# Performance work log

Hardware: AMD Instinct MI355X
Metric: run time of the kernel (lower is better)

## Reference

```python
import jax, jax.numpy as jnp
import numpy as np
import math

EPS = 1e-5


def _layernorm(x, gamma, beta):
    mu = jnp.mean(x, axis=-1, keepdims=True)
    var = jnp.mean(jnp.square(x - mu), axis=-1, keepdims=True)
    return (x - mu) * jax.lax.rsqrt(var + EPS) * gamma + beta


def setup_inputs() -> dict:
    key = jax.random.key(0)
    ks = jax.random.split(key, 8)
    B, Sq, Sk, D = 2, 2048, 2048, 1024
    s = 1.0 / math.sqrt(D)
    return {
        "Q": jax.random.normal(ks[0], (B, Sq, D), jnp.float32),
        "K": jax.random.normal(ks[1], (B, Sk, D), jnp.float32),
        "Wq": jax.random.normal(ks[2], (D, D), jnp.float32) * s,
        "bq": jnp.zeros((D,), jnp.float32),
        "Wk": jax.random.normal(ks[3], (D, D), jnp.float32) * s,
        "bk": jnp.zeros((D,), jnp.float32),
        "Wv": jax.random.normal(ks[4], (D, D), jnp.float32) * s,
        "bv": jnp.zeros((D,), jnp.float32),
        "Wo": jax.random.normal(ks[5], (D, D), jnp.float32) * s,
        "bo": jnp.zeros((D,), jnp.float32),
        "g0": jnp.ones((D,), jnp.float32),
        "b0": jnp.zeros((D,), jnp.float32),
        "g1": jnp.ones((D,), jnp.float32),
        "b1": jnp.zeros((D,), jnp.float32),
    }


def reference(Q, K, Wq, bq, Wk, bk, Wv, bv, Wo, bo, g0, b0, g1, b1):
    H = 16
    B, Sq, D = Q.shape
    dh = D // H
    Qp = Q @ Wq + bq                      # [B,Sq,D]
    Kp = K @ Wk + bk                      # [B,Sk,D]
    # Faithful to source: fc_v is applied to the ALREADY-projected K
    Vp = Kp @ Wv + bv                     # [B,Sk,D]
    # split heads: [B,S,H,dh] -> [B,H,S,dh]
    Qh = Qp.reshape(B, Sq, H, dh).transpose(0, 2, 1, 3)
    Kh = Kp.reshape(B, -1, H, dh).transpose(0, 2, 1, 3)
    Vh = Vp.reshape(B, -1, H, dh).transpose(0, 2, 1, 3)
    scores = jnp.einsum("bhqd,bhkd->bhqk", Qh, Kh) / math.sqrt(dh)
    attn = jax.nn.softmax(scores, axis=-1)  # dropout is identity in eval mode
    Oh = Qh + jnp.einsum("bhqk,bhkd->bhqd", attn, Vh)
    O = Oh.transpose(0, 2, 1, 3).reshape(B, Sq, D)
    O = _layernorm(O, g0, b0)
    O = O + jax.nn.gelu(O @ Wo + bo, approximate=False)
    O = _layernorm(O, g1, b1)
    return O
```

## Files before the change

### kernel.cpp

```cpp
#include <hip/hip_runtime.h>
#include <hip/hip_bf16.h>

typedef __attribute__((ext_vector_type(8))) short short8;
typedef __attribute__((ext_vector_type(4))) float f32x4;
typedef __attribute__((ext_vector_type(8))) unsigned short ushort8;

__device__ __forceinline__ unsigned short f32_to_bf16(float f) {
  return __builtin_bit_cast(unsigned short, __float2bfloat16(f));
}
__device__ __forceinline__ float bf16_to_f32(unsigned short u) {
  return __builtin_bit_cast(float, (unsigned)u << 16);
}

__device__ __forceinline__ void gload_lds16(const unsigned short* g, unsigned short* l) {
  __builtin_amdgcn_global_load_lds((const __attribute__((address_space(1))) void*)g,
                                   (__attribute__((address_space(3))) void*)l, 16, 0, 0);
}

__global__ __launch_bounds__(256) void transpose4_kernel(const float* __restrict__ W0,
                                                         const float* __restrict__ W1,
                                                         const float* __restrict__ W2,
                                                         const float* __restrict__ W3,
                                                         unsigned short* __restrict__ T0,
                                                         unsigned short* __restrict__ T1,
                                                         unsigned short* __restrict__ T2,
                                                         unsigned short* __restrict__ T3) {
  __shared__ float t[32][33];
  const int D = 1024;
  const float* Ws[4] = {W0, W1, W2, W3};
  unsigned short* Ts[4] = {T0, T1, T2, T3};
  const float* W = Ws[blockIdx.z];
  unsigned short* WT = Ts[blockIdx.z];
  int bx = blockIdx.x, by = blockIdx.y;
  int tx = threadIdx.x, ty = threadIdx.y;
#pragma unroll
  for (int i = 0; i < 4; ++i)
    t[ty * 4 + i][tx] = W[(size_t)(by * 32 + ty * 4 + i) * D + bx * 32 + tx];
  __syncthreads();
#pragma unroll
  for (int i = 0; i < 4; ++i) {
    int r = ty * 4 + i;
    WT[(size_t)(bx * 32 + r) * D + by * 32 + tx] = f32_to_bf16(t[tx][r]);
  }
}

template <bool GELU_RES, bool A_F32, int BK>
__device__ __forceinline__ void gemm_body(const void* __restrict__ Av,
                                          const unsigned short* __restrict__ Bt,
                                          const float* __restrict__ bias,
                                          const unsigned short* __restrict__ res16,
                                          float* __restrict__ out32,
                                          unsigned short* __restrict__ out16,
                                          unsigned short* __restrict__ outT,
                                          float o16_scale,
                                          int M, int N, int K,
                                          unsigned short* As, unsigned short* Bs) {
  const int tid = threadIdx.x;
  const int lane = tid & 63, wid = tid >> 6;
  const int wm = wid >> 2, wn = wid & 3;
  const int m0 = blockIdx.x * 64, n0 = blockIdx.y * 128;
  const int lr = lane & 15, lg = lane >> 4;
  const int xs = lr & 7;
  const int CPR = BK / 8;
  f32x4 acc[2][2] = {};
  for (int kt = 0; kt < K; kt += BK) {
#pragma unroll
    for (int i = 0; i < (128 * CPR) / 512; ++i) {
      int c = tid + i * 512;
      int r = c / CPR, pc = c % CPR;
      int lc = (pc & ~7) | ((pc & 7) ^ (r & 7));
      gload_lds16(Bt + (size_t)(n0 + r) * K + kt + lc * 8, Bs + c * 8);
    }
#pragma unroll
    for (int i = 0; i < (64 * CPR) / 512; ++i) {
      int c = tid + i * 512;
      int r = c / CPR, pc = c % CPR;
      int lc = (pc & ~7) | ((pc & 7) ^ (r & 7));
      if (A_F32) {
        const float* src = (const float*)Av + (size_t)(m0 + r) * K + kt + lc * 8;
        float4 f0 = *(const float4*)(src);
        float4 f1 = *(const float4*)(src + 4);
        ushort8 o;
        o[0] = f32_to_bf16(f0.x); o[1] = f32_to_bf16(f0.y);
        o[2] = f32_to_bf16(f0.z); o[3] = f32_to_bf16(f0.w);
        o[4] = f32_to_bf16(f1.x); o[5] = f32_to_bf16(f1.y);
        o[6] = f32_to_bf16(f1.z); o[7] = f32_to_bf16(f1.w);
        *(ushort8*)(As + c * 8) = o;
      } else {
        gload_lds16((const unsigned short*)Av + (size_t)(m0 + r) * K + kt + lc * 8,
                    As + c * 8);
      }
    }
    __syncthreads();
#pragma unroll
    for (int ks = 0; ks < BK / 32; ++ks) {
      short8 af[2], bfr[2];
      int ch = ks * 4 + lg;
      int chs = (ch & ~7) | ((ch & 7) ^ xs);
#pragma unroll
      for (int mf = 0; mf < 2; ++mf)
        af[mf] = *(const short8*)(As + (wm * 32 + mf * 16 + lr) * BK + (chs << 3));
#pragma unroll
      for (int nf = 0; nf < 2; ++nf)
        bfr[nf] = *(const short8*)(Bs + (wn * 32 + nf * 16 + lr) * BK + (chs << 3));
#pragma unroll
      for (int mf = 0; mf < 2; ++mf)
#pragma unroll
        for (int nf = 0; nf < 2; ++nf)
          acc[mf][nf] = __builtin_amdgcn_mfma_f32_16x16x32_bf16(af[mf], bfr[nf], acc[mf][nf], 0, 0, 0);
    }
    __syncthreads();
  }
#pragma unroll
  for (int nf = 0; nf < 2; ++nf) {
    int cn = n0 + wn * 32 + nf * 16 + lr;
    float bv = bias[cn];
#pragma unroll
    for (int mf = 0; mf < 2; ++mf) {
      int rm0 = m0 + wm * 32 + mf * 16 + lg * 4;
      float vv[4];
#pragma unroll
      for (int j = 0; j < 4; ++j) {
        float v = acc[mf][nf][j] + bv;
        if (GELU_RES) {
          float g = 0.5f * v * (1.0f + erff(v * 0.70710678118f));
          v = bf16_to_f32(res16[(size_t)(rm0 + j) * N + cn]) + g;
        }
        vv[j] = v;
        if (out32) out32[(size_t)(rm0 + j) * N + cn] = v;
        if (out16) out16[(size_t)(rm0 + j) * N + cn] = f32_to_bf16(v * o16_scale);
      }
      if (outT) {
        int bb = rm0 >> 11, kk = rm0 & 2047;
        int hh = cn >> 6, dd = cn & 63;
        int kin = kk & 63, kb = kk & ~63;
        int nfk = kin >> 4, lgk = (kin >> 2) & 3;
        int kperm = kb + (nfk >> 1) * 32 + lgk * 8 + (nfk & 1) * 4;
        ushort4 tv;
        tv.x = f32_to_bf16(vv[0]); tv.y = f32_to_bf16(vv[1]);
        tv.z = f32_to_bf16(vv[2]); tv.w = f32_to_bf16(vv[3]);
        *(ushort4*)(outT + ((size_t)((bb * 16 + hh) * 64 + dd)) * 2048 + kperm) = tv;
      }
    }
  }
}

template <bool GELU_RES>
__global__ __launch_bounds__(512) void gemm_kernel(const unsigned short* __restrict__ A,
                                                   const unsigned short* __restrict__ Bt,
                                                   const float* __restrict__ bias,
                                                   const unsigned short* __restrict__ res16,
                                                   float* __restrict__ out32,
                                                   unsigned short* __restrict__ out16,
                                                   unsigned short* __restrict__ outT,
                                                   int M, int N, int K) {
  __shared__ unsigned short As[64 * 128];
  __shared__ unsigned short Bs[128 * 128];
  gemm_body<GELU_RES, false, 128>(A, Bt, bias, res16, out32, out16, outT, 1.0f,
                                  M, N, K, As, Bs);
}

__global__ __launch_bounds__(512) void gemm_qk_kernel(const float* __restrict__ A0,
                                                      const float* __restrict__ A1,
                                                      const unsigned short* __restrict__ B0,
                                                      const unsigned short* __restrict__ B1,
                                                      const float* __restrict__ bias0,
                                                      const float* __restrict__ bias1,
                                                      unsigned short* __restrict__ o16_0,
                                                      unsigned short* __restrict__ o16_1,
                                                      int M, int N, int K) {
  __shared__ unsigned short As[64 * 64];
  __shared__ unsigned short Bs[128 * 64];
  int z = blockIdx.z;
  const float SCALE2 = 0.125f * 1.44269504089f;
  gemm_body<false, true, 64>(z ? (const void*)A1 : (const void*)A0, z ? B1 : B0,
                             z ? bias1 : bias0, nullptr,
                             nullptr, z ? o16_1 : o16_0, nullptr,
                             z ? 1.0f : SCALE2, M, N, K, As, Bs);
}

__global__ __launch_bounds__(512) void attn_kernel(const unsigned short* __restrict__ Qp,
                                                   const unsigned short* __restrict__ Kp,
                                                   const unsigned short* __restrict__ VpT,
                                                   unsigned short* __restrict__ O) {
  const int S = 2048, D = 1024;
  __shared__ unsigned short Ks[128 * 64];
  __shared__ unsigned short Vs[64 * 128];
  const int id = blockIdx.x;
  const int swz = (id & 7) * 64 + (id >> 3);
  const int bh = swz >> 4, qt = swz & 15;
  const int b = bh >> 4, h = bh & 15;
  const int tid = threadIdx.x, lane = tid & 63, w = tid >> 6;
  const int lr = lane & 15, lg = lane >> 4;
  const int xs = lr & 7;
  const size_t base = (size_t)(b * S) * D + h * 64;
  const size_t vbase = (size_t)(bh * 64) * S;
  const int q0 = qt * 128 + w * 16;
  const float INV_SCALE2 = 1.0f / (0.125f * 1.44269504089f);

  short8 qf[2];
#pragma unroll
  for (int ks = 0; ks < 2; ++ks)
    qf[ks] = *(const short8*)(Qp + base + (size_t)(q0 + lr) * D + ks * 32 + lg * 8);

  f32x4 oacc[4] = {};
  float m2 = -1e30f, lsum = 0.f;

  for (int kt = 0; kt < S; kt += 128) {
#pragma unroll
    for (int i = 0; i < 2; ++i) {
      int c = tid + i * 512;
      int rk = c >> 3, pck = c & 7;
      int lck = pck ^ (rk & 7);
      gload_lds16(Kp + base + (size_t)(kt + rk) * D + lck * 8, Ks + c * 8);
      int rv = c >> 4, pcv = c & 15;
      int lcv = (pcv & 8) | ((pcv & 7) ^ (rv & 7));
      gload_lds16(VpT + vbase + (size_t)rv * S + kt + lcv * 8, Vs + c * 8);
    }
    __syncthreads();

    f32x4 sacc[8];
#pragma unroll
    for (int nf = 0; nf < 8; ++nf) sacc[nf] = (f32x4){0.f, 0.f, 0.f, 0.f};
    __builtin_amdgcn_s_setprio(1);
#pragma unroll
    for (int ks = 0; ks < 2; ++ks) {
#pragma unroll
      for (int nf = 0; nf < 8; ++nf) {
        short8 kf = *(const short8*)(Ks + (nf * 16 + lr) * 64 +
                                     (((ks * 4 + lg) ^ xs) << 3));
        sacc[nf] = __builtin_amdgcn_mfma_f32_16x16x32_bf16(kf, qf[ks], sacc[nf], 0, 0, 0);
      }
    }
    __builtin_amdgcn_s_setprio(0);

    float sm = sacc[0][0];
#pragma unroll
    for (int nf = 0; nf < 8; ++nf)
#pragma unroll
      for (int r = 0; r < 4; ++r) sm = fmaxf(sm, sacc[nf][r]);
    sm = fmaxf(sm, __shfl_xor(sm, 16));
    sm = fmaxf(sm, __shfl_xor(sm, 32));
    if (__any(sm > m2 + 8.0f)) {
      float m2n = fmaxf(m2, sm);
      float alpha = __builtin_amdgcn_exp2f(m2 - m2n);
      m2 = m2n;
      lsum *= alpha;
      float a0 = __shfl(alpha, lg * 4 + 0);
      float a1 = __shfl(alpha, lg * 4 + 1);
      float a2 = __shfl(alpha, lg * 4 + 2);
      float a3 = __shfl(alpha, lg * 4 + 3);
#pragma unroll
      for (int dblk = 0; dblk < 4; ++dblk) {
        oacc[dblk][0] *= a0; oacc[dblk][1] *= a1;
        oacc[dblk][2] *= a2; oacc[dblk][3] *= a3;
      }
    }
    float rsum = 0.f;
    short8 pf[4];
#pragma unroll
    for (int nf = 0; nf < 8; ++nf) {
      float p0 = __builtin_amdgcn_exp2f(sacc[nf][0] - m2);
      float p1 = __builtin_amdgcn_exp2f(sacc[nf][1] - m2);
      float p2 = __builtin_amdgcn_exp2f(sacc[nf][2] - m2);
      float p3 = __builtin_amdgcn_exp2f(sacc[nf][3] - m2);
      rsum += (p0 + p1) + (p2 + p3);
      int ks = nf >> 1, e0 = (nf & 1) * 4;
      pf[ks][e0 + 0] = (short)f32_to_bf16(p0);
      pf[ks][e0 + 1] = (short)f32_to_bf16(p1);
      pf[ks][e0 + 2] = (short)f32_to_bf16(p2);
      pf[ks][e0 + 3] = (short)f32_to_bf16(p3);
    }
    rsum += __shfl_xor(rsum, 16);
    rsum += __shfl_xor(rsum, 32);
    lsum += rsum;

    __builtin_amdgcn_s_setprio(1);
#pragma unroll
    for (int ks = 0; ks < 4; ++ks) {
      int chs = (ks * 4 + lg);
      int chv = (chs & 8) | ((chs & 7) ^ xs);
#pragma unroll
      for (int dblk = 0; dblk < 4; ++dblk) {
        short8 vf = *(const short8*)(Vs + (dblk * 16 + lr) * 128 + (chv << 3));
        oacc[dblk] = __builtin_amdgcn_mfma_f32_16x16x32_bf16(pf[ks], vf, oacc[dblk], 0, 0, 0);
      }
    }
    __builtin_amdgcn_s_setprio(0);
    __syncthreads();
  }

  float rinv = 1.0f / lsum;
  float r0 = __shfl(rinv, lg * 4 + 0);
  float r1 = __shfl(rinv, lg * 4 + 1);
  float r2 = __shfl(rinv, lg * 4 + 2);
  float r3 = __shfl(rinv, lg * 4 + 3);
#pragma unroll
  for (int dblk = 0; dblk < 4; ++dblk) {
    float rr[4] = {r0, r1, r2, r3};
#pragma unroll
    for (int j = 0; j < 4; ++j) {
      size_t idx = base + (size_t)(q0 + lg * 4 + j) * D + dblk * 16 + lr;
      float qres = bf16_to_f32(Qp[idx]) * INV_SCALE2;
      O[idx] = f32_to_bf16(qres + oacc[dblk][j] * rr[j]);
    }
  }
}

__global__ __launch_bounds__(256) void ln_bf16_kernel(const unsigned short* __restrict__ X,
                                                      const float* __restrict__ g,
                                                      const float* __restrict__ bta,
                                                      unsigned short* __restrict__ out16,
                                                      float* __restrict__ out32) {
  const int D = 1024;
  int row = blockIdx.x;
  int t = threadIdx.x;
  ushort4 xu = *(const ushort4*)(X + (size_t)row * D + t * 4);
  float4 v;
  v.x = bf16_to_f32(xu.x); v.y = bf16_to_f32(xu.y);
  v.z = bf16_to_f32(xu.z); v.w = bf16_to_f32(xu.w);
  float s = v.x + v.y + v.z + v.w;
  float s2 = v.x * v.x + v.y * v.y + v.z * v.z + v.w * v.w;
#pragma unroll
  for (int off = 1; off < 64; off <<= 1) {
    s += __shfl_xor(s, off, 64);
    s2 += __shfl_xor(s2, off, 64);
  }
  __shared__ float red[8];
  int wid = t >> 6, lane = t & 63;
  if (lane == 0) { red[wid] = s; red[4 + wid] = s2; }
  __syncthreads();
  s = red[0] + red[1] + red[2] + red[3];
  s2 = red[4] + red[5] + red[6] + red[7];
  float mu = s * (1.f / 1024.f);
  float var = s2 * (1.f / 1024.f) - mu * mu;
  float rs = rsqrtf(var + 1e-5f);
  float4 gv = *(const float4*)(g + t * 4);
  float4 bv = *(const float4*)(bta + t * 4);
  float4 o;
  o.x = (v.x - mu) * rs * gv.x + bv.x;
  o.y = (v.y - mu) * rs * gv.y + bv.y;
  o.z = (v.z - mu) * rs * gv.z + bv.z;
  o.w = (v.w - mu) * rs * gv.w + bv.w;
  if (out16) {
    ushort4 h;
    h.x = f32_to_bf16(o.x); h.y = f32_to_bf16(o.y);
    h.z = f32_to_bf16(o.z); h.w = f32_to_bf16(o.w);
    *(ushort4*)(out16 + (size_t)row * D + t * 4) = h;
  }
  if (out32) *(float4*)(out32 + (size_t)row * D + t * 4) = o;
}

extern "C" void kernel_launch(void* const* d_in, const int* in_sizes, int n_in,
                              void* d_out, int out_size, void* d_ws, size_t ws_size,
                              hipStream_t stream) {
  const float* Q = (const float*)d_in[0];
  const float* K = (const float*)d_in[1];
  const float* Wq = (const float*)d_in[2];
  const float* bq = (const float*)d_in[3];
  const float* Wk = (const float*)d_in[4];
  const float* bk = (const float*)d_in[5];
  const float* Wv = (const float*)d_in[6];
  const float* bv = (const float*)d_in[7];
  const float* Wo = (const float*)d_in[8];
  const float* bo = (const float*)d_in[9];
  const float* g0 = (const float*)d_in[10];
  const float* b0 = (const float*)d_in[11];
  const float* g1 = (const float*)d_in[12];
  const float* b1 = (const float*)d_in[13];
  float* out = (float*)d_out;

  const int M = 4096, D = 1024;
  char* p = (char*)d_ws;
  auto alloc = [&](size_t n) { char* r = p; p += (n + 255) & ~(size_t)255; return r; };
  unsigned short* WqT = (unsigned short*)alloc((size_t)D * D * 2);
  unsigned short* WkT = (unsigned short*)alloc((size_t)D * D * 2);
  unsigned short* WvT = (unsigned short*)alloc((size_t)D * D * 2);
  unsigned short* WoT = (unsigned short*)alloc((size_t)D * D * 2);
  unsigned short* Qp16 = (unsigned short*)alloc((size_t)M * D * 2);
  unsigned short* Kp16 = (unsigned short*)alloc((size_t)M * D * 2);
  unsigned short* VpT = (unsigned short*)alloc((size_t)M * D * 2);
  unsigned short* O16 = (unsigned short*)alloc((size_t)M * D * 2);
  unsigned short* O1_16 = (unsigned short*)alloc((size_t)M * D * 2);
  unsigned short* O2_16 = (unsigned short*)alloc((size_t)M * D * 2);

  transpose4_kernel<<<dim3(32, 32, 4), dim3(32, 8), 0, stream>>>(Wq, Wk, Wv, Wo,
                                                                 WqT, WkT, WvT, WoT);

  dim3 gg(M / 64, D / 128);
  gemm_qk_kernel<<<dim3(M / 64, D / 128, 2), dim3(512), 0, stream>>>(
      Q, K, WqT, WkT, bq, bk, Qp16, Kp16, M, D, D);
  gemm_kernel<false><<<gg, dim3(512), 0, stream>>>(Kp16, WvT, bv, nullptr, nullptr, nullptr,
                                                   VpT, M, D, D);

  attn_kernel<<<dim3(512), dim3(512), 0, stream>>>(Qp16, Kp16, VpT, O16);

  ln_bf16_kernel<<<dim3(M), dim3(256), 0, stream>>>(O16, g0, b0, O1_16, nullptr);
  gemm_kernel<true><<<gg, dim3(512), 0, stream>>>(O1_16, WoT, bo, O1_16, nullptr, O2_16,
                                                  nullptr, M, D, D);
  ln_bf16_kernel<<<dim3(M), dim3(256), 0, stream>>>(O2_16, g1, b1, nullptr, out);
}
```

Before: 132.6 us.

## Split attention over key halves and fuse partial combine into first layernorm

```diff
diff --git a/kernel.cpp b/kernel.cpp
--- a/kernel.cpp
+++ b/kernel.cpp
@@ -179,16 +179,21 @@
                              z ? 1.0f : SCALE2, M, N, K, As, Bs);
 }
 
-__global__ __launch_bounds__(512) void attn_kernel(const unsigned short* __restrict__ Qp,
-                                                   const unsigned short* __restrict__ Kp,
-                                                   const unsigned short* __restrict__ VpT,
-                                                   unsigned short* __restrict__ O) {
+__global__ __launch_bounds__(512) void attn_part_kernel(const unsigned short* __restrict__ Qp,
+                                                        const unsigned short* __restrict__ Kp,
+                                                        const unsigned short* __restrict__ VpT,
+                                                        unsigned short* __restrict__ Op1,
+                                                        unsigned short* __restrict__ Op2,
+                                                        float2* __restrict__ ML1,
+                                                        float2* __restrict__ ML2) {
   const int S = 2048, D = 1024;
   __shared__ unsigned short Ks[128 * 64];
   __shared__ unsigned short Vs[64 * 128];
   const int id = blockIdx.x;
-  const int swz = (id & 7) * 64 + (id >> 3);
-  const int bh = swz >> 4, qt = swz & 15;
+  const int swz = (id & 7) * 128 + (id >> 3);
+  const int bh = swz >> 5;
+  const int qt = (swz >> 1) & 15;
+  const int kseg = swz & 1;
   const int b = bh >> 4, h = bh & 15;
   const int tid = threadIdx.x, lane = tid & 63, w = tid >> 6;
   const int lr = lane & 15, lg = lane >> 4;
@@ -196,7 +201,8 @@
   const size_t base = (size_t)(b * S) * D + h * 64;
   const size_t vbase = (size_t)(bh * 64) * S;
   const int q0 = qt * 128 + w * 16;
-  const float INV_SCALE2 = 1.0f / (0.125f * 1.44269504089f);
+  unsigned short* __restrict__ Op = kseg ? Op2 : Op1;
+  float2* __restrict__ ML = kseg ? ML2 : ML1;
 
   short8 qf[2];
 #pragma unroll
@@ -206,7 +212,8 @@
   f32x4 oacc[4] = {};
   float m2 = -1e30f, lsum = 0.f;
 
-  for (int kt = 0; kt < S; kt += 128) {
+  const int k0 = kseg * 1024;
+  for (int kt = k0; kt < k0 + 1024; kt += 128) {
 #pragma unroll
     for (int i = 0; i < 2; ++i) {
       int c = tid + i * 512;
@@ -278,7 +285,7 @@
     __builtin_amdgcn_s_setprio(1);
 #pragma unroll
     for (int ks = 0; ks < 4; ++ks) {
-      int chs = (ks * 4 + lg);
+      int chs = ks * 4 + lg;
       int chv = (chs & 8) | ((chs & 7) ^ xs);
 #pragma unroll
       for (int dblk = 0; dblk < 4; ++dblk) {
@@ -301,10 +308,67 @@
 #pragma unroll
     for (int j = 0; j < 4; ++j) {
       size_t idx = base + (size_t)(q0 + lg * 4 + j) * D + dblk * 16 + lr;
-      float qres = bf16_to_f32(Qp[idx]) * INV_SCALE2;
-      O[idx] = f32_to_bf16(qres + oacc[dblk][j] * rr[j]);
-    }
-  }
+      Op[idx] = f32_to_bf16(oacc[dblk][j] * rr[j]);
+    }
+  }
+  if (lane < 16)
+    ML[((size_t)bh << 11) + q0 + lane] = make_float2(m2, lsum);
+}
+
+__global__ __launch_bounds__(256) void combln_kernel(const unsigned short* __restrict__ Op1,
+                                                     const unsigned short* __restrict__ Op2,
+                                                     const float2* __restrict__ ML1,
+                                                     const float2* __restrict__ ML2,
+                                                     const unsigned short* __restrict__ Qp,
+                                                     const float* __restrict__ g,
+                                                     const float* __restrict__ bta,
+                                                     unsigned short* __restrict__ out16) {
+  const int D = 1024;
+  int row = blockIdx.x;
+  int t = threadIdx.x;
+  int b = row >> 11, sq = row & 2047;
+  int h = t >> 4;
+  const float INV_SCALE2 = 1.0f / (0.125f * 1.44269504089f);
+  size_t mli = (((size_t)(b * 16 + h)) << 11) + sq;
+  float2 p1 = ML1[mli], p2 = ML2[mli];
+  float m = fmaxf(p1.x, p2.x);
+  float a1 = __builtin_amdgcn_exp2f(p1.x - m) * p1.y;
+  float a2 = __builtin_amdgcn_exp2f(p2.x - m) * p2.y;
+  float wi = 1.0f / (a1 + a2);
+  a1 *= wi; a2 *= wi;
+  size_t ix = (size_t)row * D + t * 4;
+  ushort4 o1 = *(const ushort4*)(Op1 + ix);
+  ushort4 o2 = *(const ushort4*)(Op2 + ix);
+  ushort4 qu = *(const ushort4*)(Qp + ix);
+  float4 v;
+  v.x = bf16_to_f32(o1.x) * a1 + bf16_to_f32(o2.x) * a2 + bf16_to_f32(qu.x) * INV_SCALE2;
+  v.y = bf16_to_f32(o1.y) * a1 + bf16_to_f32(o2.y) * a2 + bf16_to_f32(qu.y) * INV_SCALE2;
+  v.z = bf16_to_f32(o1.z) * a1 + bf16_to_f32(o2.z) * a2 + bf16_to_f32(qu.z) * INV_SCALE2;
+  v.w = bf16_to_f32(o1.w) * a1 + bf16_to_f32(o2.w) * a2 + bf16_to_f32(qu.w) * INV_SCALE2;
+  float s = v.x + v.y + v.z + v.w;
+  float s2 = v.x * v.x + v.y * v.y + v.z * v.z + v.w * v.w;
+#pragma unroll
+  for (int off = 1; off < 64; off <<= 1) {
+    s += __shfl_xor(s, off, 64);
+    s2 += __shfl_xor(s2, off, 64);
+  }
+  __shared__ float red[8];
+  int wid = t >> 6, lane = t & 63;
+  if (lane == 0) { red[wid] = s; red[4 + wid] = s2; }
+  __syncthreads();
+  s = red[0] + red[1] + red[2] + red[3];
+  s2 = red[4] + red[5] + red[6] + red[7];
+  float mu = s * (1.f / 1024.f);
+  float var = s2 * (1.f / 1024.f) - mu * mu;
+  float rs = rsqrtf(var + 1e-5f);
+  float4 gv = *(const float4*)(g + t * 4);
+  float4 bv = *(const float4*)(bta + t * 4);
+  ushort4 hh;
+  hh.x = f32_to_bf16((v.x - mu) * rs * gv.x + bv.x);
+  hh.y = f32_to_bf16((v.y - mu) * rs * gv.y + bv.y);
+  hh.z = f32_to_bf16((v.z - mu) * rs * gv.z + bv.z);
+  hh.w = f32_to_bf16((v.w - mu) * rs * gv.w + bv.w);
+  *(ushort4*)(out16 + ix) = hh;
 }
 
 __global__ __launch_bounds__(256) void ln_bf16_kernel(const unsigned short* __restrict__ X,
@@ -380,9 +444,12 @@
   unsigned short* Qp16 = (unsigned short*)alloc((size_t)M * D * 2);
   unsigned short* Kp16 = (unsigned short*)alloc((size_t)M * D * 2);
   unsigned short* VpT = (unsigned short*)alloc((size_t)M * D * 2);
-  unsigned short* O16 = (unsigned short*)alloc((size_t)M * D * 2);
+  unsigned short* Op1 = (unsigned short*)alloc((size_t)M * D * 2);
+  unsigned short* Op2 = (unsigned short*)alloc((size_t)M * D * 2);
   unsigned short* O1_16 = (unsigned short*)alloc((size_t)M * D * 2);
   unsigned short* O2_16 = (unsigned short*)alloc((size_t)M * D * 2);
+  float2* ML1 = (float2*)alloc((size_t)M * 16 * sizeof(float2) / 16 * 16);
+  float2* ML2 = (float2*)alloc((size_t)M * 16 * sizeof(float2) / 16 * 16);
 
   transpose4_kernel<<<dim3(32, 32, 4), dim3(32, 8), 0, stream>>>(Wq, Wk, Wv, Wo,
                                                                  WqT, WkT, WvT, WoT);
@@ -393,9 +460,11 @@
   gemm_kernel<false><<<gg, dim3(512), 0, stream>>>(Kp16, WvT, bv, nullptr, nullptr, nullptr,
                                                    VpT, M, D, D);
 
-  attn_kernel<<<dim3(512), dim3(512), 0, stream>>>(Qp16, Kp16, VpT, O16);
-
-  ln_bf16_kernel<<<dim3(M), dim3(256), 0, stream>>>(O16, g0, b0, O1_16, nullptr);
+  attn_part_kernel<<<dim3(1024), dim3(512), 0, stream>>>(Qp16, Kp16, VpT,
+                                                         Op1, Op2, ML1, ML2);
+  combln_kernel<<<dim3(M), dim3(256), 0, stream>>>(Op1, Op2, ML1, ML2, Qp16,
+                                                   g0, b0, O1_16);
+
   gemm_kernel<true><<<gg, dim3(512), 0, stream>>>(O1_16, WoT, bo, O1_16, nullptr, O2_16,
                                                   nullptr, M, D, D);
   ln_bf16_kernel<<<dim3(M), dim3(256), 0, stream>>>(O2_16, g1, b1, nullptr, out);
```

Measured after the change: 136.9 us. 1.03x slower.
